# Kernel optimization log

Hardware: AMD Instinct MI355X
Metric: run time of the kernel (lower is better)

## Reference

```python
import jax, jax.numpy as jnp
import numpy as np

B, C, H, W = 8, 512, 64, 64
CQ = C // 8


def conv1x1(x, w, b):
    # x: [B,C,H,W], w: [O,C], b: [O] -> [B,O,H,W]
    return jnp.einsum('bchw,oc->bohw', x, w) + b[None, :, None, None]


def setup_inputs() -> dict:
    key = jax.random.key(0)
    ks = jax.random.split(key, 9)
    sc = 0.05
    return {
        'x2': jax.random.normal(ks[0], (B, C, H, W), jnp.float32),
        'x1': jax.random.normal(ks[1], (B, C, H, W), jnp.float32),
        'q_w': jax.random.normal(ks[2], (CQ, C), jnp.float32) * sc,
        'q_b': jax.random.normal(ks[3], (CQ,), jnp.float32) * sc,
        'k_w': jax.random.normal(ks[4], (CQ, C), jnp.float32) * sc,
        'k_b': jax.random.normal(ks[5], (CQ,), jnp.float32) * sc,
        'v_w': jax.random.normal(ks[6], (C, C), jnp.float32) * sc,
        'v_b': jax.random.normal(ks[7], (C,), jnp.float32) * sc,
        'gamma': jax.random.normal(ks[8], (1,), jnp.float32) * sc,
    }


def reference(x2, x1, q_w, q_b, k_w, k_b, v_w, v_b, gamma):
    h = x2.shape[2]
    q = conv1x1(x2, q_w, q_b)   # [B,CQ,H,W]
    k = conv1x1(x2, k_w, k_b)   # [B,CQ,H,W]
    v2 = conv1x1(x2, v_w, v_b)  # [B,C,H,W]
    v1 = conv1x1(x1, v_w, v_b)  # [B,C,H,W]

    # column (H) attention scores: query at (h,w) vs keys in same column
    energy_H = jnp.einsum('bchw,bcHw->bhwH', q, k)   # [B,H,W,H]
    # row (W) attention scores: query at (h,w) vs keys in same row
    energy_W = jnp.einsum('bchw,bchW->bhwW', q, k)   # [B,H,W,W]
    # NOTE: this module variant does NOT add the diagonal -inf mask.
    concate = jax.nn.softmax(jnp.concatenate([energy_H, energy_W], axis=3), axis=3)
    att_H = concate[..., :h]    # [B,H,W,H]
    att_W = concate[..., h:]    # [B,H,W,W]

    out_H2 = jnp.einsum('bcHw,bhwH->bchw', v2, att_H)
    out_W2 = jnp.einsum('bchW,bhwW->bchw', v2, att_W)
    out_H1 = jnp.einsum('bcHw,bhwH->bchw', v1, att_H)
    out_W1 = jnp.einsum('bchW,bhwW->bchw', v1, att_W)

    g = gamma[0]
    y2 = g * (out_H2 + out_W2) + x2
    y1 = g * (out_H1 + out_W1) + x1
    return (y2, y1)
```

## Files before the change

kernel.cpp:

```cpp
#include <hip/hip_runtime.h>
#include <cstdint>
#include <cstddef>

using u16 = unsigned short;
using u32 = unsigned int;

#define DI __device__ __forceinline__

typedef __attribute__((ext_vector_type(8))) short bf16x8;
typedef __attribute__((ext_vector_type(4))) float f32x4;

DI float bfu2f(u16 u) { return __uint_as_float(((u32)u) << 16); }
DI u16 f2bu(float f) {
    u32 x = __float_as_uint(f);
    return (u16)((x + 0x7fffu + ((x >> 16) & 1u)) >> 16);
}
DI u32 pk2(float a, float b) { return (u32)f2bu(a) | ((u32)f2bu(b) << 16); }

constexpr int CIN = 512;
constexpr int HW  = 4096;
constexpr size_t PLANE = 16777216ull;

__global__ __launch_bounds__(256) void proj_mfma(
    const float* __restrict__ X,
    const float* __restrict__ w0, const float* __restrict__ b0, int n0r,
    const float* __restrict__ w1, const float* __restrict__ b1, int n1r,
    const float* __restrict__ w2, const float* __restrict__ b2,
    u16* __restrict__ o0, u16* __restrict__ o1, u16* __restrict__ o2,
    int o0c, int o1c, int o2c)
{
    __shared__ u16 Wlds[128][40];
    __shared__ u16 Xlds[32][136];
    const int tid = threadIdx.x;
    const int m0  = blockIdx.y * 128;
    const int n0g = blockIdx.x * 128;
    const int b    = n0g >> 12;
    const int col0 = n0g & 4095;
    const float* Xb = X + (size_t)b * CIN * HW;

    const int ml = tid >> 1, wk0 = (tid & 1) * 16;
    const int xk = tid >> 3, xnb = (tid & 7) * 16;
    const int mrow = m0 + ml;
    const float* wr = (mrow < n0r) ? w0 + (size_t)mrow * CIN
                    : (mrow < n0r + n1r) ? w1 + (size_t)(mrow - n0r) * CIN
                    : w2 + (size_t)(mrow - n0r - n1r) * CIN;

    const int lane = tid & 63, wv = tid >> 6;
    const int wm = (wv & 1) * 64, wn = (wv >> 1) * 64;
    const int lr = lane & 15, lq = lane >> 4;

    f32x4 acc[4][4] = {};
    for (int kt = 0; kt < CIN; kt += 32) {
        {
            const float* p = wr + kt + wk0;
            float4 f0 = *(const float4*)(p);
            float4 f1 = *(const float4*)(p + 4);
            float4 f2 = *(const float4*)(p + 8);
            float4 f3 = *(const float4*)(p + 12);
            uint4 u0 = { pk2(f0.x, f0.y), pk2(f0.z, f0.w), pk2(f1.x, f1.y), pk2(f1.z, f1.w) };
            uint4 u1 = { pk2(f2.x, f2.y), pk2(f2.z, f2.w), pk2(f3.x, f3.y), pk2(f3.z, f3.w) };
            *(uint4*)&Wlds[ml][wk0]     = u0;
            *(uint4*)&Wlds[ml][wk0 + 8] = u1;
        }
        {
            const float* p = Xb + (size_t)(kt + xk) * HW + col0 + xnb;
            float4 f0 = *(const float4*)(p);
            float4 f1 = *(const float4*)(p + 4);
            float4 f2 = *(const float4*)(p + 8);
            float4 f3 = *(const float4*)(p + 12);
            uint4 u0 = { pk2(f0.x, f0.y), pk2(f0.z, f0.w), pk2(f1.x, f1.y), pk2(f1.z, f1.w) };
            uint4 u1 = { pk2(f2.x, f2.y), pk2(f2.z, f2.w), pk2(f3.x, f3.y), pk2(f3.z, f3.w) };
            *(uint4*)&Xlds[xk][xnb]     = u0;
            *(uint4*)&Xlds[xk][xnb + 8] = u1;
        }
        __syncthreads();
        bf16x8 a[4];
        #pragma unroll
        for (int i = 0; i < 4; i++)
            a[i] = *(const bf16x8*)&Wlds[wm + i * 16 + lr][lq * 8];
        #pragma unroll
        for (int j = 0; j < 4; j++) {
            bf16x8 bv;
            const int nn = wn + j * 16 + lr;
            #pragma unroll
            for (int jj = 0; jj < 8; jj++) bv[jj] = (short)Xlds[lq * 8 + jj][nn];
            #pragma unroll
            for (int i = 0; i < 4; i++)
                acc[i][j] = __builtin_amdgcn_mfma_f32_16x16x32_bf16(a[i], bv, acc[i][j], 0, 0, 0);
        }
        __syncthreads();
    }
    #pragma unroll
    for (int i = 0; i < 4; i++) {
        const int mbase = m0 + wm + i * 16;
        const float* bp; u16* op; int ch0, cc;
        if (mbase < n0r)             { bp = b0; op = o0; ch0 = mbase;             cc = o0c; }
        else if (mbase < n0r + n1r)  { bp = b1; op = o1; ch0 = mbase - n0r;       cc = o1c; }
        else                         { bp = b2; op = o2; ch0 = mbase - n0r - n1r; cc = o2c; }
        #pragma unroll
        for (int r = 0; r < 4; r++) {
            const int ch = ch0 + lq * 4 + r;
            const float bias = bp[ch];
            #pragma unroll
            for (int j = 0; j < 4; j++) {
                const int colx = col0 + wn + j * 16 + lr;
                op[((size_t)b * cc + ch) * HW + colx] = f2bu(acc[i][j][r] + bias);
            }
        }
    }
}

__global__ __launch_bounds__(256) void transpose64_bb(
    const u16* __restrict__ src, u16* __restrict__ dst)
{
    __shared__ u16 t[64][65];
    const size_t s = blockIdx.x;
    const u16* sp = src + s * 4096;
    u16* dp = dst + s * 4096;
    const int tid = threadIdx.x;
    #pragma unroll
    for (int i = 0; i < 16; i++) { int idx = tid + 256 * i; t[idx >> 6][idx & 63] = sp[idx]; }
    __syncthreads();
    #pragma unroll
    for (int i = 0; i < 16; i++) { int idx = tid + 256 * i; dp[idx] = t[idx & 63][idx >> 6]; }
}

__global__ __launch_bounds__(256) void transpose64_f32_inplace(float* __restrict__ d)
{
    __shared__ float t[64][65];
    float* p = d + (size_t)blockIdx.x * 4096;
    const int tid = threadIdx.x;
    #pragma unroll
    for (int i = 0; i < 16; i++) { int idx = tid + 256 * i; t[idx >> 6][idx & 63] = p[idx]; }
    __syncthreads();
    #pragma unroll
    for (int i = 0; i < 16; i++) { int idx = tid + 256 * i; p[idx] = t[idx & 63][idx >> 6]; }
}

__global__ __launch_bounds__(256) void energy_h(
    const u16* __restrict__ qT, const u16* __restrict__ kT, float* __restrict__ e)
{
    __shared__ float Qs[64][68];
    __shared__ float Ks[64][68];
    const int w = blockIdx.x, b = blockIdx.y;
    const int tid = threadIdx.x;
    const size_t base = (size_t)b * 64 * HW + (size_t)w * 64;
    #pragma unroll
    for (int i = 0; i < 16; i++) {
        int idx = tid + 256 * i;
        int c = idx >> 6, x = idx & 63;
        Qs[c][x] = bfu2f(qT[base + (size_t)c * HW + x]);
        Ks[c][x] = bfu2f(kT[base + (size_t)c * HW + x]);
    }
    __syncthreads();
    const int tx = tid & 15, ty = tid >> 4;
    float acc[4][4] = {};
    #pragma unroll 8
    for (int c = 0; c < 64; c++) {
        float4 qv = *reinterpret_cast<const float4*>(&Qs[c][tx * 4]);
        float4 kv = *reinterpret_cast<const float4*>(&Ks[c][ty * 4]);
        float a[4] = {qv.x, qv.y, qv.z, qv.w};
        float d[4] = {kv.x, kv.y, kv.z, kv.w};
        #pragma unroll
        for (int i = 0; i < 4; i++)
            #pragma unroll
            for (int j = 0; j < 4; j++) acc[i][j] += a[i] * d[j];
    }
    #pragma unroll
    for (int i = 0; i < 4; i++) {
        float4 v = make_float4(acc[i][0], acc[i][1], acc[i][2], acc[i][3]);
        *reinterpret_cast<float4*>(e + ((size_t)(b * 64 + tx * 4 + i) * 64 + w) * 128 + ty * 4) = v;
    }
}

__global__ __launch_bounds__(256) void energy_w(
    const u16* __restrict__ q, const u16* __restrict__ k, float* __restrict__ e)
{
    __shared__ float Qs[64][68];
    __shared__ float Ks[64][68];
    const int h = blockIdx.x, b = blockIdx.y;
    const int tid = threadIdx.x;
    const size_t base = (size_t)b * 64 * HW + (size_t)h * 64;
    #pragma unroll
    for (int i = 0; i < 16; i++) {
        int idx = tid + 256 * i;
        int c = idx >> 6, x = idx & 63;
        Qs[c][x] = bfu2f(q[base + (size_t)c * HW + x]);
        Ks[c][x] = bfu2f(k[base + (size_t)c * HW + x]);
    }
    __syncthreads();
    const int tx = tid & 15, ty = tid >> 4;
    float acc[4][4] = {};
    #pragma unroll 8
    for (int c = 0; c < 64; c++) {
        float4 qv = *reinterpret_cast<const float4*>(&Qs[c][tx * 4]);
        float4 kv = *reinterpret_cast<const float4*>(&Ks[c][ty * 4]);
        float a[4] = {qv.x, qv.y, qv.z, qv.w};
        float d[4] = {kv.x, kv.y, kv.z, kv.w};
        #pragma unroll
        for (int i = 0; i < 4; i++)
            #pragma unroll
            for (int j = 0; j < 4; j++) acc[i][j] += a[i] * d[j];
    }
    #pragma unroll
    for (int i = 0; i < 4; i++) {
        float4 v = make_float4(acc[i][0], acc[i][1], acc[i][2], acc[i][3]);
        *reinterpret_cast<float4*>(e + ((size_t)(b * 64 + h) * 64 + tx * 4 + i) * 128 + 64 + ty * 4) = v;
    }
}

__global__ __launch_bounds__(256) void softmax128(float* __restrict__ e)
{
    const int pos = blockIdx.x * 4 + (threadIdx.x >> 6);
    const int l = threadIdx.x & 63;
    float* p = e + (size_t)pos * 128;
    float v0 = p[l], v1 = p[l + 64];
    float m = fmaxf(v0, v1);
    #pragma unroll
    for (int o = 32; o > 0; o >>= 1) m = fmaxf(m, __shfl_xor(m, o, 64));
    float e0 = __expf(v0 - m), e1 = __expf(v1 - m);
    float s = e0 + e1;
    #pragma unroll
    for (int o = 32; o > 0; o >>= 1) s += __shfl_xor(s, o, 64);
    float inv = 1.0f / s;
    p[l] = e0 * inv;
    p[l + 64] = e1 * inv;
}

__global__ __launch_bounds__(256) void agg_h(
    const u16* __restrict__ v2T, const u16* __restrict__ v1T,
    const float* __restrict__ att, float* __restrict__ outp)
{
    __shared__ float As[64][68];
    __shared__ float Vs[64][68];
    const int ct = blockIdx.x, w = blockIdx.y, b = blockIdx.z;
    const int tid = threadIdx.x;
    #pragma unroll
    for (int i = 0; i < 16; i++) {
        int idx = tid + 256 * i;
        int hh = idx >> 6, hp = idx & 63;
        As[hp][hh] = att[((size_t)(b * 64 + hh) * 64 + w) * 128 + hp];
    }
    const int tx = tid & 15, ty = tid >> 4;
    const size_t vbase = ((size_t)(b * 512 + ct * 64) * 64 + w) * 64;
    for (int vs = 0; vs < 2; vs++) {
        const u16* vT = vs ? v1T : v2T;
        __syncthreads();
        #pragma unroll
        for (int i = 0; i < 16; i++) {
            int idx = tid + 256 * i;
            int c = idx >> 6, hp = idx & 63;
            Vs[hp][c] = bfu2f(vT[vbase + (size_t)c * 4096 + hp]);
        }
        __syncthreads();
        float acc[4][4] = {};
        #pragma unroll 8
        for (int hp = 0; hp < 64; hp++) {
            float4 vv = *reinterpret_cast<const float4*>(&Vs[hp][ty * 4]);
            float4 aa = *reinterpret_cast<const float4*>(&As[hp][tx * 4]);
            float a[4] = {vv.x, vv.y, vv.z, vv.w};
            float d[4] = {aa.x, aa.y, aa.z, aa.w};
            #pragma unroll
            for (int i = 0; i < 4; i++)
                #pragma unroll
                for (int j = 0; j < 4; j++) acc[i][j] += a[i] * d[j];
        }
        float* po = outp + (size_t)vs * PLANE;
        #pragma unroll
        for (int i = 0; i < 4; i++) {
            float4 y = make_float4(acc[i][0], acc[i][1], acc[i][2], acc[i][3]);
            *reinterpret_cast<float4*>(
                &po[((size_t)(b * 512 + ct * 64 + ty * 4 + i) * 64 + w) * 64 + tx * 4]) = y;
        }
    }
}

__global__ __launch_bounds__(256) void agg_w(
    const u16* __restrict__ v2, const u16* __restrict__ v1,
    const float* __restrict__ att,
    const float* __restrict__ x2, const float* __restrict__ x1,
    const float* __restrict__ gptr, float* __restrict__ outp)
{
    __shared__ float As[64][68];
    __shared__ float Vs[64][68];
    const int ct = blockIdx.x, h = blockIdx.y, b = blockIdx.z;
    const int tid = threadIdx.x;
    #pragma unroll
    for (int i = 0; i < 16; i++) {
        int idx = tid + 256 * i;
        int ww = idx >> 6, wp = idx & 63;
        As[wp][ww] = att[((size_t)(b * 64 + h) * 64 + ww) * 128 + 64 + wp];
    }
    const float g = gptr[0];
    const int tx = tid & 15, ty = tid >> 4;
    const size_t vbase = (size_t)(b * 512 + ct * 64) * HW + (size_t)h * 64;
    for (int vs = 0; vs < 2; vs++) {
        const u16* v = vs ? v1 : v2;
        const float* x = vs ? x1 : x2;
        float* po = outp + (size_t)vs * PLANE;
        __syncthreads();
        #pragma unroll
        for (int i = 0; i < 16; i++) {
            int idx = tid + 256 * i;
            int c = idx >> 6, wp = idx & 63;
            Vs[wp][c] = bfu2f(v[vbase + (size_t)c * HW + wp]);
        }
        __syncthreads();
        float acc[4][4] = {};
        #pragma unroll 8
        for (int wp = 0; wp < 64; wp++) {
            float4 vv = *reinterpret_cast<const float4*>(&Vs[wp][ty * 4]);
            float4 aa = *reinterpret_cast<const float4*>(&As[wp][tx * 4]);
            float a[4] = {vv.x, vv.y, vv.z, vv.w};
            float d[4] = {aa.x, aa.y, aa.z, aa.w};
            #pragma unroll
            for (int i = 0; i < 4; i++)
                #pragma unroll
                for (int j = 0; j < 4; j++) acc[i][j] += a[i] * d[j];
        }
        #pragma unroll
        for (int i = 0; i < 4; i++) {
            size_t off = (size_t)(b * 512 + ct * 64 + ty * 4 + i) * HW + (size_t)h * 64 + tx * 4;
            float4 pv = *reinterpret_cast<const float4*>(po + off);
            float4 xv = *reinterpret_cast<const float4*>(x + off);
            float4 y;
            y.x = g * (pv.x + acc[i][0]) + xv.x;
            y.y = g * (pv.y + acc[i][1]) + xv.y;
            y.z = g * (pv.z + acc[i][2]) + xv.z;
            y.w = g * (pv.w + acc[i][3]) + xv.w;
            *reinterpret_cast<float4*>(po + off) = y;
        }
    }
}

extern "C" void kernel_launch(void* const* d_in, const int* in_sizes, int n_in,
                              void* d_out, int out_size, void* d_ws, size_t ws_size,
                              hipStream_t stream)
{
    (void)in_sizes; (void)n_in; (void)out_size; (void)ws_size;
    const float* x2  = (const float*)d_in[0];
    const float* x1  = (const float*)d_in[1];
    const float* q_w = (const float*)d_in[2];
    const float* q_b = (const float*)d_in[3];
    const float* k_w = (const float*)d_in[4];
    const float* k_b = (const float*)d_in[5];
    const float* v_w = (const float*)d_in[6];
    const float* v_b = (const float*)d_in[7];
    const float* gm  = (const float*)d_in[8];

    char* ws = (char*)d_ws;
    u16*   q   = (u16*)(ws);
    u16*   k   = (u16*)(ws + ((size_t)4   << 20));
    u16*   qT  = (u16*)(ws + ((size_t)8   << 20));
    u16*   kT  = (u16*)(ws + ((size_t)12  << 20));
    float* e   = (float*)(ws + ((size_t)16 << 20));
    u16*   v2  = (u16*)(ws + ((size_t)32  << 20));
    u16*   v1  = (u16*)(ws + ((size_t)64  << 20));
    u16*   v2T = (u16*)(ws + ((size_t)96  << 20));
    u16*   v1T = (u16*)(ws + ((size_t)128 << 20));
    float* out = (float*)d_out;

    dim3 blk(256);
    proj_mfma<<<dim3(256, 5), blk, 0, stream>>>(x2, q_w, q_b, 64, k_w, k_b, 64,
                                                v_w, v_b, q, k, v2, 64, 64, 512);
    proj_mfma<<<dim3(256, 4), blk, 0, stream>>>(x1, v_w, v_b, 0, v_w, v_b, 0,
                                                v_w, v_b, q, k, v1, 64, 64, 512);
    transpose64_bb<<<1024, blk, 0, stream>>>(q, qT);
    transpose64_bb<<<8192, blk, 0, stream>>>(v2, v2T);
    energy_h<<<dim3(64, 8), blk, 0, stream>>>(qT, kT, e);
    energy_w<<<dim3(64, 8), blk, 0, stream>>>(q, k, e);
    softmax128<<<8192, blk, 0, stream>>>(e);
    agg_h<<<dim3(8, 64, 8), blk, 0, stream>>>(v2T, v1T, e, out);
    transpose64_f32_inplace<<<8192, blk, 0, stream>>>(out);
    agg_w<<<dim3(8, 64, 8), blk, 0, stream>>>(v2, v1, e, x2, x1, gm, out);
}
```

Measured before the change: 562.2 us.

## Use bf16 MFMA for attention aggregation with bf16 softmax and intermediates

```diff
diff --git a/kernel.cpp b/kernel.cpp
--- a/kernel.cpp
+++ b/kernel.cpp
@@ -125,10 +125,10 @@
     for (int i = 0; i < 16; i++) { int idx = tid + 256 * i; dp[idx] = t[idx & 63][idx >> 6]; }
 }
 
-__global__ __launch_bounds__(256) void transpose64_f32_inplace(float* __restrict__ d)
-{
-    __shared__ float t[64][65];
-    float* p = d + (size_t)blockIdx.x * 4096;
+__global__ __launch_bounds__(256) void transpose64_bb_inplace(u16* __restrict__ d)
+{
+    __shared__ u16 t[64][65];
+    u16* p = d + (size_t)blockIdx.x * 4096;
     const int tid = threadIdx.x;
     #pragma unroll
     for (int i = 0; i < 16; i++) { int idx = tid + 256 * i; t[idx >> 6][idx & 63] = p[idx]; }
@@ -209,11 +209,12 @@
     }
 }
 
-__global__ __launch_bounds__(256) void softmax128(float* __restrict__ e)
+__global__ __launch_bounds__(256) void softmax128_bf(
+    const float* __restrict__ e, u16* __restrict__ attb)
 {
     const int pos = blockIdx.x * 4 + (threadIdx.x >> 6);
     const int l = threadIdx.x & 63;
-    float* p = e + (size_t)pos * 128;
+    const float* p = e + (size_t)pos * 128;
     float v0 = p[l], v1 = p[l + 64];
     float m = fmaxf(v0, v1);
     #pragma unroll
@@ -223,114 +224,101 @@
     #pragma unroll
     for (int o = 32; o > 0; o >>= 1) s += __shfl_xor(s, o, 64);
     float inv = 1.0f / s;
-    p[l] = e0 * inv;
-    p[l + 64] = e1 * inv;
-}
-
-__global__ __launch_bounds__(256) void agg_h(
-    const u16* __restrict__ v2T, const u16* __restrict__ v1T,
-    const float* __restrict__ att, float* __restrict__ outp)
-{
-    __shared__ float As[64][68];
-    __shared__ float Vs[64][68];
-    const int ct = blockIdx.x, w = blockIdx.y, b = blockIdx.z;
-    const int tid = threadIdx.x;
-    #pragma unroll
-    for (int i = 0; i < 16; i++) {
-        int idx = tid + 256 * i;
-        int hh = idx >> 6, hp = idx & 63;
-        As[hp][hh] = att[((size_t)(b * 64 + hh) * 64 + w) * 128 + hp];
-    }
-    const int tx = tid & 15, ty = tid >> 4;
-    const size_t vbase = ((size_t)(b * 512 + ct * 64) * 64 + w) * 64;
-    for (int vs = 0; vs < 2; vs++) {
-        const u16* vT = vs ? v1T : v2T;
-        __syncthreads();
-        #pragma unroll
-        for (int i = 0; i < 16; i++) {
-            int idx = tid + 256 * i;
-            int c = idx >> 6, hp = idx & 63;
-            Vs[hp][c] = bfu2f(vT[vbase + (size_t)c * 4096 + hp]);
-        }
-        __syncthreads();
-        float acc[4][4] = {};
-        #pragma unroll 8
-        for (int hp = 0; hp < 64; hp++) {
-            float4 vv = *reinterpret_cast<const float4*>(&Vs[hp][ty * 4]);
-            float4 aa = *reinterpret_cast<const float4*>(&As[hp][tx * 4]);
-            float a[4] = {vv.x, vv.y, vv.z, vv.w};
-            float d[4] = {aa.x, aa.y, aa.z, aa.w};
+    u16* q = attb + (size_t)pos * 128;
+    q[l] = f2bu(e0 * inv);
+    q[l + 64] = f2bu(e1 * inv);
+}
+
+__global__ __launch_bounds__(256) void agg_h_mfma(
+    const u16* __restrict__ vTa, const u16* __restrict__ vTb,
+    const u16* __restrict__ attb, u16* __restrict__ Pa, u16* __restrict__ Pb)
+{
+    const int mt = blockIdx.x, w = blockIdx.y, b = blockIdx.z;
+    const u16* vT = (mt < 4) ? vTa : vTb;
+    u16*       P  = (mt < 4) ? Pa  : Pb;
+    const int c0 = (mt & 3) * 128;
+    const int lane = threadIdx.x & 63, wv = threadIdx.x >> 6;
+    const int wm = (wv & 1) * 64, wn = (wv >> 1) * 32;
+    const int lr = lane & 15, lq = lane >> 4;
+    const u16* va = vT + ((size_t)(b * 512 + c0) * 64 + w) * 64;
+    const u16* ab = attb + ((size_t)b * 4096 + w) * 128;
+    bf16x8 afr[2][4], bfr[2][2];
+    #pragma unroll
+    for (int kt = 0; kt < 2; kt++) {
+        const int k0 = kt * 32 + lq * 8;
+        #pragma unroll
+        for (int i = 0; i < 4; i++)
+            afr[kt][i] = *(const bf16x8*)(va + (size_t)(wm + i * 16 + lr) * 4096 + k0);
+        #pragma unroll
+        for (int j = 0; j < 2; j++)
+            bfr[kt][j] = *(const bf16x8*)(ab + (size_t)(wn + j * 16 + lr) * 8192 + k0);
+    }
+    __syncthreads();
+    f32x4 acc[4][2] = {};
+    #pragma unroll
+    for (int kt = 0; kt < 2; kt++)
+        #pragma unroll
+        for (int j = 0; j < 2; j++)
             #pragma unroll
             for (int i = 0; i < 4; i++)
-                #pragma unroll
-                for (int j = 0; j < 4; j++) acc[i][j] += a[i] * d[j];
-        }
-        float* po = outp + (size_t)vs * PLANE;
-        #pragma unroll
-        for (int i = 0; i < 4; i++) {
-            float4 y = make_float4(acc[i][0], acc[i][1], acc[i][2], acc[i][3]);
-            *reinterpret_cast<float4*>(
-                &po[((size_t)(b * 512 + ct * 64 + ty * 4 + i) * 64 + w) * 64 + tx * 4]) = y;
-        }
-    }
-}
-
-__global__ __launch_bounds__(256) void agg_w(
+                acc[i][j] = __builtin_amdgcn_mfma_f32_16x16x32_bf16(afr[kt][i], bfr[kt][j], acc[i][j], 0, 0, 0);
+    #pragma unroll
+    for (int i = 0; i < 4; i++)
+        #pragma unroll
+        for (int j = 0; j < 2; j++) {
+            u16* pp = P + ((size_t)(b * 512 + c0 + wm + i * 16 + lq * 4) * 64 + w) * 64 + wn + j * 16 + lr;
+            #pragma unroll
+            for (int r = 0; r < 4; r++) pp[(size_t)r * 4096] = f2bu(acc[i][j][r]);
+        }
+}
+
+__global__ __launch_bounds__(256) void agg_w_mfma(
     const u16* __restrict__ v2, const u16* __restrict__ v1,
-    const float* __restrict__ att,
+    const u16* __restrict__ P2, const u16* __restrict__ P1,
+    const u16* __restrict__ attb,
     const float* __restrict__ x2, const float* __restrict__ x1,
-    const float* __restrict__ gptr, float* __restrict__ outp)
-{
-    __shared__ float As[64][68];
-    __shared__ float Vs[64][68];
-    const int ct = blockIdx.x, h = blockIdx.y, b = blockIdx.z;
-    const int tid = threadIdx.x;
-    #pragma unroll
-    for (int i = 0; i < 16; i++) {
-        int idx = tid + 256 * i;
-        int ww = idx >> 6, wp = idx & 63;
-        As[wp][ww] = att[((size_t)(b * 64 + h) * 64 + ww) * 128 + 64 + wp];
+    const float* __restrict__ gptr, float* __restrict__ out)
+{
+    const int mt = blockIdx.x, h = blockIdx.y, b = blockIdx.z;
+    const u16* v = (mt < 4) ? v2 : v1;
+    const u16* P = (mt < 4) ? P2 : P1;
+    const float* x = (mt < 4) ? x2 : x1;
+    float* y = out + ((mt < 4) ? 0 : PLANE);
+    const int c0 = (mt & 3) * 128;
+    const int lane = threadIdx.x & 63, wv = threadIdx.x >> 6;
+    const int wm = (wv & 1) * 64, wn = (wv >> 1) * 32;
+    const int lr = lane & 15, lq = lane >> 4;
+    const u16* vb = v + (size_t)(b * 512 + c0) * 4096 + h * 64;
+    const u16* ab = attb + ((size_t)(b * 64 + h) * 64) * 128 + 64;
+    f32x4 acc[4][2] = {};
+    #pragma unroll
+    for (int kt = 0; kt < 2; kt++) {
+        const int k0 = kt * 32 + lq * 8;
+        bf16x8 afr[4];
+        #pragma unroll
+        for (int i = 0; i < 4; i++)
+            afr[i] = *(const bf16x8*)(vb + (size_t)(wm + i * 16 + lr) * 4096 + k0);
+        #pragma unroll
+        for (int j = 0; j < 2; j++) {
+            bf16x8 bfr = *(const bf16x8*)(ab + (size_t)(wn + j * 16 + lr) * 128 + k0);
+            #pragma unroll
+            for (int i = 0; i < 4; i++)
+                acc[i][j] = __builtin_amdgcn_mfma_f32_16x16x32_bf16(afr[i], bfr, acc[i][j], 0, 0, 0);
+        }
     }
     const float g = gptr[0];
-    const int tx = tid & 15, ty = tid >> 4;
-    const size_t vbase = (size_t)(b * 512 + ct * 64) * HW + (size_t)h * 64;
-    for (int vs = 0; vs < 2; vs++) {
-        const u16* v = vs ? v1 : v2;
-        const float* x = vs ? x1 : x2;
-        float* po = outp + (size_t)vs * PLANE;
-        __syncthreads();
-        #pragma unroll
-        for (int i = 0; i < 16; i++) {
-            int idx = tid + 256 * i;
-            int c = idx >> 6, wp = idx & 63;
-            Vs[wp][c] = bfu2f(v[vbase + (size_t)c * HW + wp]);
-        }
-        __syncthreads();
-        float acc[4][4] = {};
-        #pragma unroll 8
-        for (int wp = 0; wp < 64; wp++) {
-            float4 vv = *reinterpret_cast<const float4*>(&Vs[wp][ty * 4]);
-            float4 aa = *reinterpret_cast<const float4*>(&As[wp][tx * 4]);
-            float a[4] = {vv.x, vv.y, vv.z, vv.w};
-            float d[4] = {aa.x, aa.y, aa.z, aa.w};
-            #pragma unroll
-            for (int i = 0; i < 4; i++)
-                #pragma unroll
-                for (int j = 0; j < 4; j++) acc[i][j] += a[i] * d[j];
-        }
-        #pragma unroll
-        for (int i = 0; i < 4; i++) {
-            size_t off = (size_t)(b * 512 + ct * 64 + ty * 4 + i) * HW + (size_t)h * 64 + tx * 4;
-            float4 pv = *reinterpret_cast<const float4*>(po + off);
-            float4 xv = *reinterpret_cast<const float4*>(x + off);
-            float4 y;
-            y.x = g * (pv.x + acc[i][0]) + xv.x;
-            y.y = g * (pv.y + acc[i][1]) + xv.y;
-            y.z = g * (pv.z + acc[i][2]) + xv.z;
-            y.w = g * (pv.w + acc[i][3]) + xv.w;
-            *reinterpret_cast<float4*>(po + off) = y;
-        }
-    }
+    #pragma unroll
+    for (int i = 0; i < 4; i++)
+        #pragma unroll
+        for (int j = 0; j < 2; j++) {
+            size_t off = (size_t)(b * 512 + c0 + wm + i * 16 + lq * 4) * 4096
+                       + (size_t)h * 64 + wn + j * 16 + lr;
+            #pragma unroll
+            for (int r = 0; r < 4; r++) {
+                size_t o = off + (size_t)r * 4096;
+                y[o] = g * (bfu2f(P[o]) + acc[i][j][r]) + x[o];
+            }
+        }
 }
 
 extern "C" void kernel_launch(void* const* d_in, const int* in_sizes, int n_in,
@@ -349,15 +337,16 @@
     const float* gm  = (const float*)d_in[8];
 
     char* ws = (char*)d_ws;
-    u16*   q   = (u16*)(ws);
-    u16*   k   = (u16*)(ws + ((size_t)4   << 20));
-    u16*   qT  = (u16*)(ws + ((size_t)8   << 20));
-    u16*   kT  = (u16*)(ws + ((size_t)12  << 20));
-    float* e   = (float*)(ws + ((size_t)16 << 20));
-    u16*   v2  = (u16*)(ws + ((size_t)32  << 20));
-    u16*   v1  = (u16*)(ws + ((size_t)64  << 20));
-    u16*   v2T = (u16*)(ws + ((size_t)96  << 20));
-    u16*   v1T = (u16*)(ws + ((size_t)128 << 20));
+    u16*   v2   = (u16*)(ws);
+    u16*   v1   = (u16*)(ws + ((size_t)32  << 20));
+    u16*   attb = (u16*)(ws + ((size_t)64  << 20));
+    u16*   q    = (u16*)(ws + ((size_t)72  << 20));
+    u16*   k    = (u16*)(ws + ((size_t)76  << 20));
+    u16*   qT   = (u16*)(ws + ((size_t)80  << 20));
+    u16*   kT   = (u16*)(ws + ((size_t)84  << 20));
+    float* e    = (float*)(ws + ((size_t)88 << 20));
+    u16*   vT2  = (u16*)(ws + ((size_t)72  << 20));
+    u16*   vT1  = (u16*)(ws + ((size_t)104 << 20));
     float* out = (float*)d_out;
 
     dim3 blk(256);
@@ -366,11 +355,12 @@
     proj_mfma<<<dim3(256, 4), blk, 0, stream>>>(x1, v_w, v_b, 0, v_w, v_b, 0,
                                                 v_w, v_b, q, k, v1, 64, 64, 512);
     transpose64_bb<<<1024, blk, 0, stream>>>(q, qT);
-    transpose64_bb<<<8192, blk, 0, stream>>>(v2, v2T);
     energy_h<<<dim3(64, 8), blk, 0, stream>>>(qT, kT, e);
     energy_w<<<dim3(64, 8), blk, 0, stream>>>(q, k, e);
-    softmax128<<<8192, blk, 0, stream>>>(e);
-    agg_h<<<dim3(8, 64, 8), blk, 0, stream>>>(v2T, v1T, e, out);
-    transpose64_f32_inplace<<<8192, blk, 0, stream>>>(out);
-    agg_w<<<dim3(8, 64, 8), blk, 0, stream>>>(v2, v1, e, x2, x1, gm, out);
-}
+    softmax128_bf<<<8192, blk, 0, stream>>>(e, attb);
+    transpose64_bb<<<8192, blk, 0, stream>>>(v2, vT2);
+    agg_h_mfma<<<dim3(8, 64, 8), blk, 0, stream>>>(vT2, vT1, attb, vT2, vT1);
+    transpose64_bb_inplace<<<8192, blk, 0, stream>>>(vT2);
+    agg_w_mfma<<<dim3(8, 64, 8), blk, 0, stream>>>(v2, v1, vT2, vT1, attb,
+                                                   x2, x1, gm, out);
+}
```

After: 589.9 us. 4.9% more time.
